# Optimization experiments

Measured on AMD Instinct MI355X. Metric: run time of the kernel, lower is better.

The kernel has to match this reference:

```python
import jax, jax.numpy as jnp
import numpy as np

NEG_INF = -1e9


def setup_inputs() -> dict:
    key = jax.random.key(0)
    ks = jax.random.split(key, 10)
    B, S, D, H = 16, 1024, 256, 4
    dk = D // H  # 64
    q = jax.random.normal(ks[0], (B, S, D), jnp.float32)
    k = jax.random.normal(ks[1], (B, S, D), jnp.float32)
    v = jax.random.normal(ks[2], (B, S, D), jnp.float32)
    # causal mask: True where attention is disallowed (future positions)
    mask = jnp.triu(jnp.ones((S, S), bool), k=1)
    # parameters (torch Linear stored as [in, out]); xavier-uniform, zero bias
    def xav(kk, shape):
        fan_in, fan_out = shape[-2], shape[-1]
        lim = jnp.sqrt(6.0 / (fan_in + fan_out))
        return jax.random.uniform(kk, shape, jnp.float32, -lim, lim)
    Wv = xav(ks[3], (D, dk)); bv = jnp.zeros((dk,), jnp.float32)
    Wq = xav(ks[4], (H, D, dk)); bq = jnp.zeros((H, dk), jnp.float32)
    Wk = xav(ks[5], (H, D, dk)); bk = jnp.zeros((H, dk), jnp.float32)
    Wh = xav(ks[6], (dk, D))  # w_h, no bias
    return {"q": q, "k": k, "v": v, "mask": mask,
            "Wq": Wq, "bq": bq, "Wk": Wk, "bk": bk,
            "Wv": Wv, "bv": bv, "Wh": Wh}


def reference(q, k, v, mask, Wq, bq, Wk, bk, Wv, bv, Wh):
    dk = Wv.shape[-1]
    scale = 1.0 / jnp.sqrt(jnp.asarray(dk, q.dtype))
    vs = v @ Wv + bv                                   # [B,S,dk] shared V
    qs = jnp.einsum('bsd,hdk->bhsk', q, Wq) + bq[None, :, None, :]
    kk = jnp.einsum('bsd,hdk->bhsk', k, Wk) + bk[None, :, None, :]
    scores = jnp.einsum('bhsk,bhtk->bhst', qs, kk) * scale  # [B,H,S,S]
    scores = jnp.where(mask[None, None, :, :], NEG_INF, scores)
    attn = jax.nn.softmax(scores, axis=-1)             # [B,H,S,S]
    head = jnp.einsum('bhst,btk->bhsk', attn, vs)      # [B,H,S,dk]
    outputs = jnp.mean(head, axis=1)                   # mean over heads [B,S,dk]
    outputs = outputs @ Wh                             # [B,S,D]
    return outputs, attn
```

## Files before the change

kernel.cpp:

```cpp
#include <hip/hip_runtime.h>

typedef __attribute__((ext_vector_type(8))) short short8;
typedef __attribute__((ext_vector_type(4))) float floatx4;

#define MFMA_BF16(a, b, c) __builtin_amdgcn_mfma_f32_16x16x32_bf16((a), (b), (c), 0, 0, 0)

static __device__ __forceinline__ unsigned short f2bf(float f) {
  unsigned u = __builtin_bit_cast(unsigned, f);
  u += 0x7FFFu + ((u >> 16) & 1u);
  return (unsigned short)(u >> 16);
}
static __device__ __forceinline__ short f2bf_s(float f) { return (short)f2bf(f); }
static __device__ __forceinline__ float bf2f(unsigned short s) {
  unsigned u = ((unsigned)s) << 16;
  return __builtin_bit_cast(float, u);
}

__global__ __launch_bounds__(256) void k_prep(
    const float* __restrict__ Wq, const float* __restrict__ Wk,
    const float* __restrict__ Wv, const float* __restrict__ Wh,
    unsigned short* __restrict__ wqt_hi, unsigned short* __restrict__ wqt_lo,
    unsigned short* __restrict__ wkt_hi, unsigned short* __restrict__ wkt_lo,
    unsigned short* __restrict__ wvt, unsigned short* __restrict__ wht) {
  int idx = blockIdx.x * 256 + threadIdx.x;
  int d = idx & 255, c = (idx >> 8) & 63, h = idx >> 14;
  float qv = Wq[(h * 256 + d) * 64 + c];
  float kv = Wk[(h * 256 + d) * 64 + c];
  unsigned short qh = f2bf(qv);
  wqt_hi[idx] = qh;
  wqt_lo[idx] = f2bf(qv - bf2f(qh));
  unsigned short kh = f2bf(kv);
  wkt_hi[idx] = kh;
  wkt_lo[idx] = f2bf(kv - bf2f(kh));
  if (idx < 64 * 256) {
    int dd = idx & 255, cc = idx >> 8;
    wvt[idx] = f2bf(Wv[dd * 64 + cc]);
    int d2 = idx & 63, oc = idx >> 6;
    wht[idx] = f2bf(Wh[d2 * 256 + oc]);
  }
}

static __device__ __forceinline__ void proj_one(
    const float* __restrict__ xr,
    const unsigned short* __restrict__ wt_hi, const unsigned short* __restrict__ wt_lo,
    const float* __restrict__ bias,
    unsigned short* __restrict__ o_hi, unsigned short* __restrict__ o_lo,
    int b, int sbase, int lane) {
  int lr = lane & 15, lg = lane >> 4, kb = lg * 8;
  short8 ahi[8], alo[8];
#pragma unroll
  for (int ks = 0; ks < 8; ++ks) {
    floatx4 f0 = *(const floatx4*)(xr + ks * 32 + kb);
    floatx4 f1 = *(const floatx4*)(xr + ks * 32 + kb + 4);
#pragma unroll
    for (int e = 0; e < 4; ++e) {
      unsigned short h0 = f2bf(f0[e]);
      ahi[ks][e] = (short)h0;
      alo[ks][e] = f2bf_s(f0[e] - bf2f(h0));
      unsigned short h1 = f2bf(f1[e]);
      ahi[ks][e + 4] = (short)h1;
      alo[ks][e + 4] = f2bf_s(f1[e] - bf2f(h1));
    }
  }
#pragma unroll 4
  for (int ct = 0; ct < 16; ++ct) {
    int col = ct * 16 + lr;
    const unsigned short* bh = wt_hi + col * 256 + kb;
    const unsigned short* bl = wt_lo + col * 256 + kb;
    floatx4 acc = {0.f, 0.f, 0.f, 0.f};
#pragma unroll
    for (int ks = 0; ks < 8; ++ks) {
      short8 wbh = *(const short8*)(bh + ks * 32);
      short8 wbl = *(const short8*)(bl + ks * 32);
      acc = MFMA_BF16(ahi[ks], wbh, acc);
      acc = MFMA_BF16(alo[ks], wbh, acc);
      acc = MFMA_BF16(ahi[ks], wbl, acc);
    }
    int hh = col >> 6, c = col & 63;
    float bs = bias[col];
#pragma unroll
    for (int j = 0; j < 4; ++j) {
      float val = acc[j] + bs;
      unsigned short hi = f2bf(val);
      size_t o = (((size_t)b * 4 + hh) * 1024 + (size_t)(sbase + lg * 4 + j)) * 64 + c;
      o_hi[o] = hi;
      o_lo[o] = f2bf(val - bf2f(hi));
    }
  }
}

__global__ __launch_bounds__(256) void k_proj(
    const float* __restrict__ q, const float* __restrict__ k, const float* __restrict__ v,
    const float* __restrict__ bq, const float* __restrict__ bk, const float* __restrict__ bv,
    const unsigned short* __restrict__ wqt_hi, const unsigned short* __restrict__ wqt_lo,
    const unsigned short* __restrict__ wkt_hi, const unsigned short* __restrict__ wkt_lo,
    const unsigned short* __restrict__ wvt,
    unsigned short* __restrict__ qs_hi, unsigned short* __restrict__ qs_lo,
    unsigned short* __restrict__ kk_hi, unsigned short* __restrict__ kk_lo,
    unsigned short* __restrict__ vst) {
  int w = threadIdx.x >> 6, lane = threadIdx.x & 63;
  int gstrip = blockIdx.x * 64 + w * 16;
  int b = gstrip >> 10, sbase = gstrip & 1023;
  int lr = lane & 15, lg = lane >> 4, kb = lg * 8;

  proj_one(q + (size_t)(gstrip + lr) * 256, wqt_hi, wqt_lo, bq, qs_hi, qs_lo, b, sbase, lane);
  proj_one(k + (size_t)(gstrip + lr) * 256, wkt_hi, wkt_lo, bk, kk_hi, kk_lo, b, sbase, lane);

  __shared__ unsigned short vtile[4][16][66];
  {
    const float* xr = v + (size_t)(gstrip + lr) * 256;
    short8 av[8];
#pragma unroll
    for (int ks = 0; ks < 8; ++ks) {
      floatx4 f0 = *(const floatx4*)(xr + ks * 32 + kb);
      floatx4 f1 = *(const floatx4*)(xr + ks * 32 + kb + 4);
#pragma unroll
      for (int e = 0; e < 4; ++e) { av[ks][e] = f2bf_s(f0[e]); av[ks][e + 4] = f2bf_s(f1[e]); }
    }
#pragma unroll
    for (int ct = 0; ct < 4; ++ct) {
      int col = ct * 16 + lr;
      floatx4 acc = {0.f, 0.f, 0.f, 0.f};
#pragma unroll
      for (int ks = 0; ks < 8; ++ks) {
        short8 wb = *(const short8*)(wvt + col * 256 + ks * 32 + kb);
        acc = MFMA_BF16(av[ks], wb, acc);
      }
      float bs = bv[col];
#pragma unroll
      for (int j = 0; j < 4; ++j) vtile[w][lg * 4 + j][col] = f2bf(acc[j] + bs);
    }
  }
  __syncthreads();
  {
    short8 t0, t1;
#pragma unroll
    for (int r = 0; r < 8; ++r) t0[r] = (short)vtile[w][r][lane];
#pragma unroll
    for (int r = 0; r < 8; ++r) t1[r] = (short)vtile[w][r + 8][lane];
    unsigned short* dst = vst + ((size_t)b * 64 + lane) * 1024 + sbase;
    *(short8*)dst = t0;
    *(short8*)(dst + 8) = t1;
  }
}

__global__ __launch_bounds__(256) void k_attn(
    const unsigned short* __restrict__ qs_hi, const unsigned short* __restrict__ qs_lo,
    const unsigned short* __restrict__ kk_hi, const unsigned short* __restrict__ kk_lo,
    const unsigned short* __restrict__ vst,
    float* __restrict__ attn, float* __restrict__ head) {
  const float SCL = 0.18033688011112042f;
  int h = blockIdx.y, b = blockIdx.z;
  int w = threadIdx.x >> 6, lane = threadIdx.x & 63;
  int lr = lane & 15, lg = lane >> 4, kb = lg * 8;
  __shared__ float plds[4][16][68];

  const unsigned short* kbh = kk_hi + ((size_t)b * 4 + h) * 65536;
  const unsigned short* kbl = kk_lo + ((size_t)b * 4 + h) * 65536;
  const unsigned short* vbb = vst + (size_t)b * 65536;

  for (int qsel = 0; qsel < 2; ++qsel) {
    int qt = qsel ? (15 - (int)blockIdx.x) : (int)blockIdx.x;
    int strip = qt * 64 + w * 16;

    short8 qah[2], qal[2];
    {
      size_t qoff = (((size_t)b * 4 + h) * 1024 + strip + lr) * 64 + kb;
      qah[0] = *(const short8*)(qs_hi + qoff);
      qah[1] = *(const short8*)(qs_hi + qoff + 32);
      qal[0] = *(const short8*)(qs_lo + qoff);
      qal[1] = *(const short8*)(qs_lo + qoff + 32);
    }

    float m[4], l[4];
#pragma unroll
    for (int j = 0; j < 4; ++j) { m[j] = -INFINITY; l[j] = 0.f; }

    for (int kt = 0; kt <= qt; ++kt) {
      floatx4 sc[4];
#pragma unroll
      for (int ct = 0; ct < 4; ++ct) {
        int kr = kt * 64 + ct * 16 + lr;
        const unsigned short* kph = kbh + (size_t)kr * 64 + kb;
        const unsigned short* kpl = kbl + (size_t)kr * 64 + kb;
        floatx4 acc = {0.f, 0.f, 0.f, 0.f};
#pragma unroll
        for (int ks = 0; ks < 2; ++ks) {
          short8 bhv = *(const short8*)(kph + ks * 32);
          short8 blv = *(const short8*)(kpl + ks * 32);
          acc = MFMA_BF16(qah[ks], bhv, acc);
          acc = MFMA_BF16(qal[ks], bhv, acc);
          acc = MFMA_BF16(qah[ks], blv, acc);
        }
#pragma unroll
        for (int j = 0; j < 4; ++j) sc[ct][j] = acc[j] * SCL;
      }
      if (kt == qt) {
#pragma unroll
        for (int ct = 0; ct < 4; ++ct)
#pragma unroll
          for (int j = 0; j < 4; ++j)
            if (kt * 64 + ct * 16 + lr > strip + lg * 4 + j) sc[ct][j] = -INFINITY;
      }
      float mx[4], ss[4];
#pragma unroll
      for (int j = 0; j < 4; ++j)
        mx[j] = fmaxf(fmaxf(sc[0][j], sc[1][j]), fmaxf(sc[2][j], sc[3][j]));
#pragma unroll
      for (int off = 1; off < 16; off <<= 1)
#pragma unroll
        for (int j = 0; j < 4; ++j) mx[j] = fmaxf(mx[j], __shfl_xor(mx[j], off));
#pragma unroll
      for (int j = 0; j < 4; ++j) {
        float mn = fmaxf(m[j], mx[j]);
        ss[j] = exp2f(sc[0][j] - mn) + exp2f(sc[1][j] - mn) +
                exp2f(sc[2][j] - mn) + exp2f(sc[3][j] - mn);
        mx[j] = mn;
      }
#pragma unroll
      for (int off = 1; off < 16; off <<= 1)
#pragma unroll
        for (int j = 0; j < 4; ++j) ss[j] += __shfl_xor(ss[j], off);
#pragma unroll
      for (int j = 0; j < 4; ++j) {
        l[j] = l[j] * exp2f(m[j] - mx[j]) + ss[j];
        m[j] = mx[j];
      }
    }

    float linv[4];
#pragma unroll
    for (int j = 0; j < 4; ++j) linv[j] = 1.0f / l[j];

    floatx4 hacc[4];
#pragma unroll
    for (int dt = 0; dt < 4; ++dt) hacc[dt] = (floatx4){0.f, 0.f, 0.f, 0.f};

    float* arow = attn + (((size_t)b * 4 + h) * 1024 + strip) * 1024;

    for (int kt = 0; kt <= qt; ++kt) {
      floatx4 sc[4];
#pragma unroll
      for (int ct = 0; ct < 4; ++ct) {
        int kr = kt * 64 + ct * 16 + lr;
        const unsigned short* kph = kbh + (size_t)kr * 64 + kb;
        const unsigned short* kpl = kbl + (size_t)kr * 64 + kb;
        floatx4 acc = {0.f, 0.f, 0.f, 0.f};
#pragma unroll
        for (int ks = 0; ks < 2; ++ks) {
          short8 bhv = *(const short8*)(kph + ks * 32);
          short8 blv = *(const short8*)(kpl + ks * 32);
          acc = MFMA_BF16(qah[ks], bhv, acc);
          acc = MFMA_BF16(qal[ks], bhv, acc);
          acc = MFMA_BF16(qah[ks], blv, acc);
        }
#pragma unroll
        for (int j = 0; j < 4; ++j) sc[ct][j] = acc[j] * SCL;
      }
      if (kt == qt) {
#pragma unroll
        for (int ct = 0; ct < 4; ++ct)
#pragma unroll
          for (int j = 0; j < 4; ++j)
            if (kt * 64 + ct * 16 + lr > strip + lg * 4 + j) sc[ct][j] = -INFINITY;
      }
#pragma unroll
      for (int ct = 0; ct < 4; ++ct)
#pragma unroll
        for (int j = 0; j < 4; ++j)
          plds[w][lg * 4 + j][ct * 16 + lr] = exp2f(sc[ct][j] - m[j]) * linv[j];
      __syncthreads();
#pragma unroll
      for (int i = 0; i < 4; ++i) {
        int rowl = lg + i * 4;
        floatx4 pv = *(const floatx4*)&plds[w][rowl][lr * 4];
        *(floatx4*)(arow + (size_t)rowl * 1024 + kt * 64 + lr * 4) = pv;
      }
#pragma unroll
      for (int ks = 0; ks < 2; ++ks) {
        floatx4 p0 = *(const floatx4*)&plds[w][lr][ks * 32 + kb];
        floatx4 p1 = *(const floatx4*)&plds[w][lr][ks * 32 + kb + 4];
        short8 pa;
#pragma unroll
        for (int e = 0; e < 4; ++e) { pa[e] = f2bf_s(p0[e]); pa[e + 4] = f2bf_s(p1[e]); }
        const unsigned short* vp = vbb + kt * 64 + ks * 32 + kb;
#pragma unroll
        for (int dt = 0; dt < 4; ++dt) {
          short8 vb = *(const short8*)(vp + (size_t)(dt * 16 + lr) * 1024);
          hacc[dt] = MFMA_BF16(pa, vb, hacc[dt]);
        }
      }
    }

#pragma unroll
    for (int dt = 0; dt < 4; ++dt)
#pragma unroll
      for (int j = 0; j < 4; ++j)
        head[(((size_t)b * 1024 + strip + lg * 4 + j) * 4 + h) * 64 + dt * 16 + lr] = hacc[dt][j];

    floatx4 z = {0.f, 0.f, 0.f, 0.f};
    for (int kt = qt + 1; kt < 16; ++kt)
#pragma unroll
      for (int i = 0; i < 4; ++i)
        *(floatx4*)(arow + (size_t)(lg + i * 4) * 1024 + kt * 64 + lr * 4) = z;
  }
}

__global__ __launch_bounds__(256) void k_out(
    const float* __restrict__ head, const unsigned short* __restrict__ wht,
    float* __restrict__ out) {
  int w = threadIdx.x >> 6, lane = threadIdx.x & 63;
  int lr = lane & 15, lg = lane >> 4, kb = lg * 8;
  int gstrip = blockIdx.x * 64 + w * 16;
  short8 a[2];
  const float* hrow = head + (size_t)(gstrip + lr) * 256;
#pragma unroll
  for (int ks = 0; ks < 2; ++ks) {
    float s8[8];
#pragma unroll
    for (int e = 0; e < 8; ++e) s8[e] = 0.f;
#pragma unroll
    for (int hh = 0; hh < 4; ++hh) {
      const float* p = hrow + hh * 64 + ks * 32 + kb;
      floatx4 f0 = *(const floatx4*)p;
      floatx4 f1 = *(const floatx4*)(p + 4);
#pragma unroll
      for (int e = 0; e < 4; ++e) { s8[e] += f0[e]; s8[e + 4] += f1[e]; }
    }
#pragma unroll
    for (int e = 0; e < 8; ++e) a[ks][e] = f2bf_s(s8[e] * 0.25f);
  }
#pragma unroll 4
  for (int ct = 0; ct < 16; ++ct) {
    int col = ct * 16 + lr;
    floatx4 acc = {0.f, 0.f, 0.f, 0.f};
#pragma unroll
    for (int ks = 0; ks < 2; ++ks) {
      short8 wb = *(const short8*)(wht + col * 64 + ks * 32 + kb);
      acc = MFMA_BF16(a[ks], wb, acc);
    }
#pragma unroll
    for (int j = 0; j < 4; ++j)
      out[(size_t)(gstrip + lg * 4 + j) * 256 + col] = acc[j];
  }
}

extern "C" void kernel_launch(void* const* d_in, const int* in_sizes, int n_in,
                              void* d_out, int out_size, void* d_ws, size_t ws_size,
                              hipStream_t stream) {
  (void)in_sizes; (void)n_in; (void)out_size; (void)ws_size;
  const float* q  = (const float*)d_in[0];
  const float* k  = (const float*)d_in[1];
  const float* v  = (const float*)d_in[2];
  const float* Wq = (const float*)d_in[4];
  const float* bq = (const float*)d_in[5];
  const float* Wk = (const float*)d_in[6];
  const float* bk = (const float*)d_in[7];
  const float* Wv = (const float*)d_in[8];
  const float* bv = (const float*)d_in[9];
  const float* Wh = (const float*)d_in[10];

  float* outp = (float*)d_out;
  float* attn = outp + (size_t)16 * 1024 * 256;

  char* wsc = (char*)d_ws;
  unsigned short* wqt_hi = (unsigned short*)(wsc + 0);
  unsigned short* wqt_lo = (unsigned short*)(wsc + 131072);
  unsigned short* wkt_hi = (unsigned short*)(wsc + 262144);
  unsigned short* wkt_lo = (unsigned short*)(wsc + 393216);
  unsigned short* wvt    = (unsigned short*)(wsc + 524288);
  unsigned short* wht    = (unsigned short*)(wsc + 557056);
  unsigned short* qsh    = (unsigned short*)(wsc + 589824);
  unsigned short* qsl    = (unsigned short*)(wsc + 8978432);
  unsigned short* kkh    = (unsigned short*)(wsc + 17367040);
  unsigned short* kkl    = (unsigned short*)(wsc + 25755648);
  unsigned short* vstp   = (unsigned short*)(wsc + 34144256);
  float*          headp  = (float*)(wsc + 36241408);

  k_prep<<<dim3(256), dim3(256), 0, stream>>>(Wq, Wk, Wv, Wh, wqt_hi, wqt_lo,
                                              wkt_hi, wkt_lo, wvt, wht);
  k_proj<<<dim3(256), dim3(256), 0, stream>>>(q, k, v, bq, bk, bv, wqt_hi, wqt_lo,
                                              wkt_hi, wkt_lo, wvt, qsh, qsl, kkh, kkl, vstp);
  k_attn<<<dim3(8, 4, 16), dim3(256), 0, stream>>>(qsh, qsl, kkh, kkl, vstp, attn, headp);
  k_out<<<dim3(256), dim3(256), 0, stream>>>(headp, wht, outp);
}
```

Before: 575.8 us.

## Stage projection and output stores through LDS, split attention into one tile per block

```diff
diff --git a/kernel.cpp b/kernel.cpp
--- a/kernel.cpp
+++ b/kernel.cpp
@@ -45,7 +45,7 @@
     const unsigned short* __restrict__ wt_hi, const unsigned short* __restrict__ wt_lo,
     const float* __restrict__ bias,
     unsigned short* __restrict__ o_hi, unsigned short* __restrict__ o_lo,
-    int b, int sbase, int lane) {
+    int b, int sbase, int lane, unsigned short (*tile)[16][264]) {
   int lr = lane & 15, lg = lane >> 4, kb = lg * 8;
   short8 ahi[8], alo[8];
 #pragma unroll
@@ -76,15 +76,28 @@
       acc = MFMA_BF16(alo[ks], wbh, acc);
       acc = MFMA_BF16(ahi[ks], wbl, acc);
     }
-    int hh = col >> 6, c = col & 63;
     float bs = bias[col];
 #pragma unroll
     for (int j = 0; j < 4; ++j) {
       float val = acc[j] + bs;
       unsigned short hi = f2bf(val);
-      size_t o = (((size_t)b * 4 + hh) * 1024 + (size_t)(sbase + lg * 4 + j)) * 64 + c;
-      o_hi[o] = hi;
-      o_lo[o] = f2bf(val - bf2f(hi));
+      tile[0][lg * 4 + j][col] = hi;
+      tile[1][lg * 4 + j][col] = f2bf(val - bf2f(hi));
+    }
+  }
+#pragma unroll
+  for (int hl = 0; hl < 2; ++hl) {
+    unsigned short* dstb = hl ? o_lo : o_hi;
+#pragma unroll
+    for (int hh = 0; hh < 4; ++hh) {
+      unsigned short* region = dstb + (((size_t)b * 4 + hh) * 1024 + sbase) * 64;
+#pragma unroll
+      for (int i = 0; i < 2; ++i) {
+        int chunk = i * 64 + lane;
+        int r = chunk >> 3, c = (chunk & 7) * 8;
+        short8 vv = *(const short8*)&tile[hl][r][hh * 64 + c];
+        *(short8*)(region + chunk * 8) = vv;
+      }
     }
   }
 }
@@ -103,10 +116,12 @@
   int b = gstrip >> 10, sbase = gstrip & 1023;
   int lr = lane & 15, lg = lane >> 4, kb = lg * 8;
 
-  proj_one(q + (size_t)(gstrip + lr) * 256, wqt_hi, wqt_lo, bq, qs_hi, qs_lo, b, sbase, lane);
-  proj_one(k + (size_t)(gstrip + lr) * 256, wkt_hi, wkt_lo, bk, kk_hi, kk_lo, b, sbase, lane);
-
-  __shared__ unsigned short vtile[4][16][66];
+  __shared__ unsigned short stile[4][2][16][264];
+  unsigned short (*tile)[16][264] = stile[w];
+
+  proj_one(q + (size_t)(gstrip + lr) * 256, wqt_hi, wqt_lo, bq, qs_hi, qs_lo, b, sbase, lane, tile);
+  proj_one(k + (size_t)(gstrip + lr) * 256, wkt_hi, wkt_lo, bk, kk_hi, kk_lo, b, sbase, lane, tile);
+
   {
     const float* xr = v + (size_t)(gstrip + lr) * 256;
     short8 av[8];
@@ -128,16 +143,13 @@
       }
       float bs = bv[col];
 #pragma unroll
-      for (int j = 0; j < 4; ++j) vtile[w][lg * 4 + j][col] = f2bf(acc[j] + bs);
-    }
-  }
-  __syncthreads();
-  {
+      for (int j = 0; j < 4; ++j) tile[0][lg * 4 + j][col] = f2bf(acc[j] + bs);
+    }
     short8 t0, t1;
 #pragma unroll
-    for (int r = 0; r < 8; ++r) t0[r] = (short)vtile[w][r][lane];
-#pragma unroll
-    for (int r = 0; r < 8; ++r) t1[r] = (short)vtile[w][r + 8][lane];
+    for (int r = 0; r < 8; ++r) t0[r] = (short)tile[0][r][lane];
+#pragma unroll
+    for (int r = 0; r < 8; ++r) t1[r] = (short)tile[0][r + 8][lane];
     unsigned short* dst = vst + ((size_t)b * 64 + lane) * 1024 + sbase;
     *(short8*)dst = t0;
     *(short8*)(dst + 8) = t1;
@@ -151,6 +163,7 @@
     float* __restrict__ attn, float* __restrict__ head) {
   const float SCL = 0.18033688011112042f;
   int h = blockIdx.y, b = blockIdx.z;
+  int qt = 15 - (int)blockIdx.x;
   int w = threadIdx.x >> 6, lane = threadIdx.x & 63;
   int lr = lane & 15, lg = lane >> 4, kb = lg * 8;
   __shared__ float plds[4][16][68];
@@ -159,150 +172,154 @@
   const unsigned short* kbl = kk_lo + ((size_t)b * 4 + h) * 65536;
   const unsigned short* vbb = vst + (size_t)b * 65536;
 
-  for (int qsel = 0; qsel < 2; ++qsel) {
-    int qt = qsel ? (15 - (int)blockIdx.x) : (int)blockIdx.x;
-    int strip = qt * 64 + w * 16;
-
-    short8 qah[2], qal[2];
-    {
-      size_t qoff = (((size_t)b * 4 + h) * 1024 + strip + lr) * 64 + kb;
-      qah[0] = *(const short8*)(qs_hi + qoff);
-      qah[1] = *(const short8*)(qs_hi + qoff + 32);
-      qal[0] = *(const short8*)(qs_lo + qoff);
-      qal[1] = *(const short8*)(qs_lo + qoff + 32);
-    }
-
-    float m[4], l[4];
-#pragma unroll
-    for (int j = 0; j < 4; ++j) { m[j] = -INFINITY; l[j] = 0.f; }
-
-    for (int kt = 0; kt <= qt; ++kt) {
-      floatx4 sc[4];
-#pragma unroll
-      for (int ct = 0; ct < 4; ++ct) {
-        int kr = kt * 64 + ct * 16 + lr;
-        const unsigned short* kph = kbh + (size_t)kr * 64 + kb;
-        const unsigned short* kpl = kbl + (size_t)kr * 64 + kb;
-        floatx4 acc = {0.f, 0.f, 0.f, 0.f};
-#pragma unroll
-        for (int ks = 0; ks < 2; ++ks) {
-          short8 bhv = *(const short8*)(kph + ks * 32);
-          short8 blv = *(const short8*)(kpl + ks * 32);
-          acc = MFMA_BF16(qah[ks], bhv, acc);
-          acc = MFMA_BF16(qal[ks], bhv, acc);
-          acc = MFMA_BF16(qah[ks], blv, acc);
-        }
-#pragma unroll
-        for (int j = 0; j < 4; ++j) sc[ct][j] = acc[j] * SCL;
-      }
-      if (kt == qt) {
-#pragma unroll
-        for (int ct = 0; ct < 4; ++ct)
-#pragma unroll
-          for (int j = 0; j < 4; ++j)
-            if (kt * 64 + ct * 16 + lr > strip + lg * 4 + j) sc[ct][j] = -INFINITY;
-      }
-      float mx[4], ss[4];
-#pragma unroll
-      for (int j = 0; j < 4; ++j)
-        mx[j] = fmaxf(fmaxf(sc[0][j], sc[1][j]), fmaxf(sc[2][j], sc[3][j]));
-#pragma unroll
-      for (int off = 1; off < 16; off <<= 1)
-#pragma unroll
-        for (int j = 0; j < 4; ++j) mx[j] = fmaxf(mx[j], __shfl_xor(mx[j], off));
-#pragma unroll
-      for (int j = 0; j < 4; ++j) {
-        float mn = fmaxf(m[j], mx[j]);
-        ss[j] = exp2f(sc[0][j] - mn) + exp2f(sc[1][j] - mn) +
-                exp2f(sc[2][j] - mn) + exp2f(sc[3][j] - mn);
-        mx[j] = mn;
-      }
-#pragma unroll
-      for (int off = 1; off < 16; off <<= 1)
-#pragma unroll
-        for (int j = 0; j < 4; ++j) ss[j] += __shfl_xor(ss[j], off);
-#pragma unroll
-      for (int j = 0; j < 4; ++j) {
-        l[j] = l[j] * exp2f(m[j] - mx[j]) + ss[j];
-        m[j] = mx[j];
-      }
-    }
-
-    float linv[4];
-#pragma unroll
-    for (int j = 0; j < 4; ++j) linv[j] = 1.0f / l[j];
-
-    floatx4 hacc[4];
-#pragma unroll
-    for (int dt = 0; dt < 4; ++dt) hacc[dt] = (floatx4){0.f, 0.f, 0.f, 0.f};
-
-    float* arow = attn + (((size_t)b * 4 + h) * 1024 + strip) * 1024;
-
-    for (int kt = 0; kt <= qt; ++kt) {
-      floatx4 sc[4];
-#pragma unroll
-      for (int ct = 0; ct < 4; ++ct) {
-        int kr = kt * 64 + ct * 16 + lr;
-        const unsigned short* kph = kbh + (size_t)kr * 64 + kb;
-        const unsigned short* kpl = kbl + (size_t)kr * 64 + kb;
-        floatx4 acc = {0.f, 0.f, 0.f, 0.f};
-#pragma unroll
-        for (int ks = 0; ks < 2; ++ks) {
-          short8 bhv = *(const short8*)(kph + ks * 32);
-          short8 blv = *(const short8*)(kpl + ks * 32);
-          acc = MFMA_BF16(qah[ks], bhv, acc);
-          acc = MFMA_BF16(qal[ks], bhv, acc);
-          acc = MFMA_BF16(qah[ks], blv, acc);
-        }
-#pragma unroll
-        for (int j = 0; j < 4; ++j) sc[ct][j] = acc[j] * SCL;
-      }
-      if (kt == qt) {
-#pragma unroll
-        for (int ct = 0; ct < 4; ++ct)
-#pragma unroll
-          for (int j = 0; j < 4; ++j)
-            if (kt * 64 + ct * 16 + lr > strip + lg * 4 + j) sc[ct][j] = -INFINITY;
-      }
-#pragma unroll
-      for (int ct = 0; ct < 4; ++ct)
-#pragma unroll
-        for (int j = 0; j < 4; ++j)
-          plds[w][lg * 4 + j][ct * 16 + lr] = exp2f(sc[ct][j] - m[j]) * linv[j];
-      __syncthreads();
-#pragma unroll
-      for (int i = 0; i < 4; ++i) {
-        int rowl = lg + i * 4;
-        floatx4 pv = *(const floatx4*)&plds[w][rowl][lr * 4];
-        *(floatx4*)(arow + (size_t)rowl * 1024 + kt * 64 + lr * 4) = pv;
-      }
-#pragma unroll
-      for (int ks = 0; ks < 2; ++ks) {
-        floatx4 p0 = *(const floatx4*)&plds[w][lr][ks * 32 + kb];
-        floatx4 p1 = *(const floatx4*)&plds[w][lr][ks * 32 + kb + 4];
-        short8 pa;
-#pragma unroll
-        for (int e = 0; e < 4; ++e) { pa[e] = f2bf_s(p0[e]); pa[e + 4] = f2bf_s(p1[e]); }
-        const unsigned short* vp = vbb + kt * 64 + ks * 32 + kb;
-#pragma unroll
-        for (int dt = 0; dt < 4; ++dt) {
-          short8 vb = *(const short8*)(vp + (size_t)(dt * 16 + lr) * 1024);
-          hacc[dt] = MFMA_BF16(pa, vb, hacc[dt]);
-        }
-      }
-    }
-
-#pragma unroll
-    for (int dt = 0; dt < 4; ++dt)
-#pragma unroll
-      for (int j = 0; j < 4; ++j)
-        head[(((size_t)b * 1024 + strip + lg * 4 + j) * 4 + h) * 64 + dt * 16 + lr] = hacc[dt][j];
-
+  int strip = qt * 64 + w * 16;
+  float* arow = attn + (((size_t)b * 4 + h) * 1024 + strip) * 1024;
+
+  {
     floatx4 z = {0.f, 0.f, 0.f, 0.f};
     for (int kt = qt + 1; kt < 16; ++kt)
 #pragma unroll
       for (int i = 0; i < 4; ++i)
         *(floatx4*)(arow + (size_t)(lg + i * 4) * 1024 + kt * 64 + lr * 4) = z;
+  }
+
+  short8 qah[2], qal[2];
+  {
+    size_t qoff = (((size_t)b * 4 + h) * 1024 + strip + lr) * 64 + kb;
+    qah[0] = *(const short8*)(qs_hi + qoff);
+    qah[1] = *(const short8*)(qs_hi + qoff + 32);
+    qal[0] = *(const short8*)(qs_lo + qoff);
+    qal[1] = *(const short8*)(qs_lo + qoff + 32);
+  }
+
+  float m[4], l[4];
+#pragma unroll
+  for (int j = 0; j < 4; ++j) { m[j] = -INFINITY; l[j] = 0.f; }
+
+  for (int kt = 0; kt <= qt; ++kt) {
+    floatx4 sc[4];
+#pragma unroll
+    for (int ct = 0; ct < 4; ++ct) {
+      int kr = kt * 64 + ct * 16 + lr;
+      const unsigned short* kph = kbh + (size_t)kr * 64 + kb;
+      const unsigned short* kpl = kbl + (size_t)kr * 64 + kb;
+      floatx4 acc = {0.f, 0.f, 0.f, 0.f};
+#pragma unroll
+      for (int ks = 0; ks < 2; ++ks) {
+        short8 bhv = *(const short8*)(kph + ks * 32);
+        short8 blv = *(const short8*)(kpl + ks * 32);
+        acc = MFMA_BF16(qah[ks], bhv, acc);
+        acc = MFMA_BF16(qal[ks], bhv, acc);
+        acc = MFMA_BF16(qah[ks], blv, acc);
+      }
+#pragma unroll
+      for (int j = 0; j < 4; ++j) sc[ct][j] = acc[j] * SCL;
+    }
+    if (kt == qt) {
+#pragma unroll
+      for (int ct = 0; ct < 4; ++ct)
+#pragma unroll
+        for (int j = 0; j < 4; ++j)
+          if (kt * 64 + ct * 16 + lr > strip + lg * 4 + j) sc[ct][j] = -INFINITY;
+    }
+    float mx[4], ss[4];
+#pragma unroll
+    for (int j = 0; j < 4; ++j)
+      mx[j] = fmaxf(fmaxf(sc[0][j], sc[1][j]), fmaxf(sc[2][j], sc[3][j]));
+#pragma unroll
+    for (int off = 1; off < 16; off <<= 1)
+#pragma unroll
+      for (int j = 0; j < 4; ++j) mx[j] = fmaxf(mx[j], __shfl_xor(mx[j], off));
+#pragma unroll
+    for (int j = 0; j < 4; ++j) {
+      float mn = fmaxf(m[j], mx[j]);
+      ss[j] = exp2f(sc[0][j] - mn) + exp2f(sc[1][j] - mn) +
+              exp2f(sc[2][j] - mn) + exp2f(sc[3][j] - mn);
+      mx[j] = mn;
+    }
+#pragma unroll
+    for (int off = 1; off < 16; off <<= 1)
+#pragma unroll
+      for (int j = 0; j < 4; ++j) ss[j] += __shfl_xor(ss[j], off);
+#pragma unroll
+    for (int j = 0; j < 4; ++j) {
+      l[j] = l[j] * exp2f(m[j] - mx[j]) + ss[j];
+      m[j] = mx[j];
+    }
+  }
+
+  float linv[4];
+#pragma unroll
+  for (int j = 0; j < 4; ++j) linv[j] = 1.0f / l[j];
+
+  floatx4 hacc[4];
+#pragma unroll
+  for (int dt = 0; dt < 4; ++dt) hacc[dt] = (floatx4){0.f, 0.f, 0.f, 0.f};
+
+  for (int kt = 0; kt <= qt; ++kt) {
+    floatx4 sc[4];
+#pragma unroll
+    for (int ct = 0; ct < 4; ++ct) {
+      int kr = kt * 64 + ct * 16 + lr;
+      const unsigned short* kph = kbh + (size_t)kr * 64 + kb;
+      const unsigned short* kpl = kbl + (size_t)kr * 64 + kb;
+      floatx4 acc = {0.f, 0.f, 0.f, 0.f};
+#pragma unroll
+      for (int ks = 0; ks < 2; ++ks) {
+        short8 bhv = *(const short8*)(kph + ks * 32);
+        short8 blv = *(const short8*)(kpl + ks * 32);
+        acc = MFMA_BF16(qah[ks], bhv, acc);
+        acc = MFMA_BF16(qal[ks], bhv, acc);
+        acc = MFMA_BF16(qah[ks], blv, acc);
+      }
+#pragma unroll
+      for (int j = 0; j < 4; ++j) sc[ct][j] = acc[j] * SCL;
+    }
+    if (kt == qt) {
+#pragma unroll
+      for (int ct = 0; ct < 4; ++ct)
+#pragma unroll
+        for (int j = 0; j < 4; ++j)
+          if (kt * 64 + ct * 16 + lr > strip + lg * 4 + j) sc[ct][j] = -INFINITY;
+    }
+#pragma unroll
+    for (int ct = 0; ct < 4; ++ct)
+#pragma unroll
+      for (int j = 0; j < 4; ++j)
+        plds[w][lg * 4 + j][ct * 16 + lr] = exp2f(sc[ct][j] - m[j]) * linv[j];
+#pragma unroll
+    for (int i = 0; i < 4; ++i) {
+      int rowl = lg + i * 4;
+      floatx4 pv = *(const floatx4*)&plds[w][rowl][lr * 4];
+      *(floatx4*)(arow + (size_t)rowl * 1024 + kt * 64 + lr * 4) = pv;
+    }
+#pragma unroll
+    for (int ks = 0; ks < 2; ++ks) {
+      floatx4 p0 = *(const floatx4*)&plds[w][lr][ks * 32 + kb];
+      floatx4 p1 = *(const floatx4*)&plds[w][lr][ks * 32 + kb + 4];
+      short8 pa;
+#pragma unroll
+      for (int e = 0; e < 4; ++e) { pa[e] = f2bf_s(p0[e]); pa[e + 4] = f2bf_s(p1[e]); }
+      const unsigned short* vp = vbb + kt * 64 + ks * 32 + kb;
+#pragma unroll
+      for (int dt = 0; dt < 4; ++dt) {
+        short8 vb = *(const short8*)(vp + (size_t)(dt * 16 + lr) * 1024);
+        hacc[dt] = MFMA_BF16(pa, vb, hacc[dt]);
+      }
+    }
+  }
+
+#pragma unroll
+  for (int dt = 0; dt < 4; ++dt)
+#pragma unroll
+    for (int j = 0; j < 4; ++j)
+      plds[w][lg * 4 + j][dt * 16 + lr] = hacc[dt][j];
+#pragma unroll
+  for (int i = 0; i < 4; ++i) {
+    int chunk = i * 64 + lane;
+    int r = chunk >> 4, c = (chunk & 15) * 4;
+    floatx4 vv = *(const floatx4*)&plds[w][r][c];
+    *(floatx4*)(head + (((size_t)b * 1024 + strip + r) * 4 + h) * 64 + c) = vv;
   }
 }
 
@@ -312,6 +329,8 @@
   int w = threadIdx.x >> 6, lane = threadIdx.x & 63;
   int lr = lane & 15, lg = lane >> 4, kb = lg * 8;
   int gstrip = blockIdx.x * 64 + w * 16;
+  int cy = blockIdx.y;
+  __shared__ float otile[4][16][132];
   short8 a[2];
   const float* hrow = head + (size_t)(gstrip + lr) * 256;
 #pragma unroll
@@ -330,9 +349,9 @@
 #pragma unroll
     for (int e = 0; e < 8; ++e) a[ks][e] = f2bf_s(s8[e] * 0.25f);
   }
-#pragma unroll 4
-  for (int ct = 0; ct < 16; ++ct) {
-    int col = ct * 16 + lr;
+#pragma unroll
+  for (int ct = 0; ct < 8; ++ct) {
+    int col = cy * 128 + ct * 16 + lr;
     floatx4 acc = {0.f, 0.f, 0.f, 0.f};
 #pragma unroll
     for (int ks = 0; ks < 2; ++ks) {
@@ -340,8 +359,14 @@
       acc = MFMA_BF16(a[ks], wb, acc);
     }
 #pragma unroll
-    for (int j = 0; j < 4; ++j)
-      out[(size_t)(gstrip + lg * 4 + j) * 256 + col] = acc[j];
+    for (int j = 0; j < 4; ++j) otile[w][lg * 4 + j][ct * 16 + lr] = acc[j];
+  }
+#pragma unroll
+  for (int i = 0; i < 8; ++i) {
+    int chunk = i * 64 + lane;
+    int r = chunk >> 5, c = (chunk & 31) * 4;
+    floatx4 vv = *(const floatx4*)&otile[w][r][c];
+    *(floatx4*)(out + (size_t)(gstrip + r) * 256 + cy * 128 + c) = vv;
   }
 }
 
@@ -381,6 +406,6 @@
                                               wkt_hi, wkt_lo, wvt, wht);
   k_proj<<<dim3(256), dim3(256), 0, stream>>>(q, k, v, bq, bk, bv, wqt_hi, wqt_lo,
                                               wkt_hi, wkt_lo, wvt, qsh, qsl, kkh, kkl, vstp);
-  k_attn<<<dim3(8, 4, 16), dim3(256), 0, stream>>>(qsh, qsl, kkh, kkl, vstp, attn, headp);
-  k_out<<<dim3(256), dim3(256), 0, stream>>>(headp, wht, outp);
-}
+  k_attn<<<dim3(16, 4, 16), dim3(256), 0, stream>>>(qsh, qsl, kkh, kkl, vstp, attn, headp);
+  k_out<<<dim3(256, 2), dim3(256), 0, stream>>>(headp, wht, outp);
+}
```

Result: slower. 668.9 us (+16.2%).
